# Kernel optimization log

Measured on AMD Instinct MI355X. Metric: run time of the kernel, lower is better.

Reference implementation:

```python
import jax, jax.numpy as jnp
import numpy as np

B, S, D = 4, 4096, 1024
H = 16
HD = D // H
L = 4
MLP_MULT = 4
MAX_CHUNKS = 1024
ROPE_BASE = 10000.0


def _rms(x):
    eps = jnp.asarray(jnp.finfo(x.dtype).eps, x.dtype)
    return x * jax.lax.rsqrt(jnp.mean(x * x, axis=-1, keepdims=True) + eps)


def _rope_tables(seq_len, dim):
    inv = 1.0 / ROPE_BASE ** (np.arange(0, dim, 2, dtype=np.float32) / dim)
    t = np.arange(seq_len, dtype=np.float32)
    freqs = np.outer(t, inv)  # [T, dim/2]
    return jnp.asarray(np.cos(freqs)), jnp.asarray(np.sin(freqs))


def _apply_rope(x, cos, sin):
    # x: [B,H,T,hd]; cos/sin: [T, hd/2]
    half = x.shape[-1] // 2
    x1, x2 = x[..., :half], x[..., half:]
    c = cos[None, None, :, :]
    s = sin[None, None, :, :]
    return jnp.concatenate([x1 * c + x2 * s, -x1 * s + x2 * c], axis=-1)


def chunk_reduce(x, boundary_hard, max_chunks):
    # x: [B,S,D]; boundary_hard: [B,S] in {0,1}, boundary_hard[:,0]==1
    ids = jnp.cumsum(boundary_hard.astype(jnp.int32), axis=1) - 1  # [B,S]
    seg = lambda xb, ib: jax.ops.segment_sum(xb, ib, num_segments=max_chunks)
    sums = jax.vmap(seg)(x, ids)                                   # [B,C,D]
    counts = jax.vmap(seg)(jnp.ones(x.shape[:2], x.dtype)[..., None].swapaxes(0, 0), ids) if False else jax.vmap(seg)(jnp.ones((x.shape[0], x.shape[1], 1), x.dtype), ids)
    latents = sums / jnp.maximum(counts, 1.0)
    num_chunks = ids[:, -1] + 1
    valid = jnp.arange(max_chunks)[None, :] < num_chunks[:, None]
    return latents, ids, valid


def _attn(x, wq, wk, wv, wo, qg, cos, sin):
    b, t, _ = x.shape
    q = (x @ wq.T).reshape(b, t, H, HD).transpose(0, 2, 1, 3)
    k = (x @ wk.T).reshape(b, t, H, HD).transpose(0, 2, 1, 3)
    v = (x @ wv.T).reshape(b, t, H, HD).transpose(0, 2, 1, 3)
    q = _apply_rope(_rms(q), cos, sin)
    k = _apply_rope(_rms(k), cos, sin)
    q = q * qg[None, :, None, None]
    scores = jnp.einsum('bhqd,bhkd->bhqk', q, k) / np.sqrt(HD).astype(np.float32)
    causal = jnp.tril(jnp.ones((t, t), bool))
    scores = jnp.where(causal[None, None], scores, jnp.asarray(-jnp.inf, scores.dtype))
    p = jax.nn.softmax(scores, axis=-1)
    y = jnp.einsum('bhqk,bhkd->bhqd', p, v).transpose(0, 2, 1, 3).reshape(b, t, D)
    return y @ wo.T


def _mlp(x, fc, proj):
    h = jax.nn.relu(x @ fc.T)
    return (h * h) @ proj.T


def reference(x, boundary_hard, Wq, Wk, Wv, Wo, q_gain, fc_w, proj_w,
              attn_scale, mlp_scale, resid_mix, max_chunks):
    latents, _, valid = chunk_reduce(x, boundary_hard, max_chunks)
    cos, sin = _rope_tables(max_chunks, HD)
    x0 = latents
    h = latents
    for l in range(L):
        mix = resid_mix[l]
        h = mix[0][None, None, :] * h + mix[1][None, None, :] * x0
        a = _attn(_rms(h), Wq[l], Wk[l], Wv[l], Wo[l], q_gain[l], cos, sin)
        h = h + attn_scale[l][None, None, :] * a
        h = h + mlp_scale[l][None, None, :] * _mlp(_rms(h), fc_w[l], proj_w[l])
    return h * valid[..., None].astype(h.dtype)


def setup_inputs() -> dict:
    key = jax.random.key(0)
    ks = jax.random.split(key, 12)
    rng = np.random.default_rng(0)
    boundary = np.zeros((B, S), np.int32)
    for b in range(B):
        kcnt = int(rng.integers(MAX_CHUNKS // 2, MAX_CHUNKS - 1))
        pos = rng.choice(S, size=kcnt, replace=False)
        boundary[b, pos] = 1
    boundary[:, 0] = 1
    sd = 0.02
    return {
        'x': jax.random.normal(ks[0], (B, S, D), jnp.float32),
        'boundary_hard': jnp.asarray(boundary),
        'Wq': jax.random.normal(ks[1], (L, D, D), jnp.float32) * sd,
        'Wk': jax.random.normal(ks[2], (L, D, D), jnp.float32) * sd,
        'Wv': jax.random.normal(ks[3], (L, D, D), jnp.float32) * sd,
        'Wo': jax.random.normal(ks[4], (L, D, D), jnp.float32) * sd,
        'q_gain': jnp.ones((L, H), jnp.float32),
        'fc_w': jax.random.normal(ks[5], (L, MLP_MULT * D, D), jnp.float32) * sd,
        'proj_w': jax.random.normal(ks[6], (L, D, MLP_MULT * D), jnp.float32) * sd,
        'attn_scale': jnp.ones((L, D), jnp.float32),
        'mlp_scale': jnp.ones((L, D), jnp.float32),
        'resid_mix': jnp.stack([jnp.ones((L, D)), jnp.zeros((L, D))], axis=1).astype(jnp.float32),
        'max_chunks': MAX_CHUNKS,
    }
```

## Files before the change

### kernel.cpp

```cpp
#include <hip/hip_runtime.h>
#include <math.h>

#define BB   4
#define SS   4096
#define DD   1024
#define HH   16
#define HDIM 64
#define CC   1024
#define DFF  4096
#define LL   4

static constexpr float F32_EPS = 1.1920928955078125e-07f;

typedef __attribute__((ext_vector_type(8))) __bf16 bf16x8;
typedef __attribute__((ext_vector_type(4))) float  f32x4;

__device__ __forceinline__ uint f2bf(float f) {
    uint u = __float_as_uint(f);
    return (u + 0x7fffu + ((u >> 16) & 1u)) >> 16;
}
__device__ __forceinline__ float bf2f(uint u) {
    return __uint_as_float(u << 16);
}

__device__ __forceinline__ void gl_lds16(const ushort* g, ushort* l) {
    __builtin_amdgcn_global_load_lds(
        (const __attribute__((address_space(1))) unsigned int*)g,
        (__attribute__((address_space(3))) unsigned int*)l, 16, 0, 0);
}

__global__ __launch_bounds__(256) void castlayer_kernel(const float* __restrict__ Wq,
                                                        const float* __restrict__ Wk,
                                                        const float* __restrict__ Wv,
                                                        const float* __restrict__ Wo,
                                                        const float* __restrict__ fc,
                                                        const float* __restrict__ proj,
                                                        ushort* __restrict__ out) {
    int i = blockIdx.x * blockDim.x + threadIdx.x;
    const int U = DD * DD / 8;
    const float* src;
    if (i < 3 * U) {
        src = (i < U ? Wq : (i < 2 * U ? Wk : Wv)) + (size_t)(i < U ? i : (i < 2*U ? i-U : i-2*U)) * 8;
    } else if (i < 4 * U) {
        src = Wo + (size_t)(i - 3 * U) * 8;
    } else if (i < 8 * U) {
        src = fc + (size_t)(i - 4 * U) * 8;
    } else {
        src = proj + (size_t)(i - 8 * U) * 8;
    }
    const float4* p = (const float4*)src;
    float4 a = p[0], b = p[1];
    uint4 o;
    o.x = f2bf(a.x) | (f2bf(a.y) << 16);
    o.y = f2bf(a.z) | (f2bf(a.w) << 16);
    o.z = f2bf(b.x) | (f2bf(b.y) << 16);
    o.w = f2bf(b.z) | (f2bf(b.w) << 16);
    *(uint4*)(out + (size_t)i * 8) = o;
}

__global__ void rope_init_kernel(float* __restrict__ cosT, float* __restrict__ sinT) {
    int idx = blockIdx.x * blockDim.x + threadIdx.x;
    int pos = idx >> 5;
    int i   = idx & 31;
    float inv = powf(10000.0f, -(float)i / 32.0f);
    float f = (float)pos * inv;
    cosT[idx] = cosf(f);
    sinT[idx] = sinf(f);
}

__global__ __launch_bounds__(1024) void scan_kernel(const int* __restrict__ boundary,
                                                    int* __restrict__ starts,
                                                    int* __restrict__ nch) {
    __shared__ int tmp[1024];
    int b = blockIdx.x, t = threadIdx.x;
    int base = b * SS + t * 4;
    int v0 = boundary[base + 0], v1 = boundary[base + 1];
    int v2 = boundary[base + 2], v3 = boundary[base + 3];
    int p0 = v0, p1 = p0 + v1, p2 = p1 + v2, p3 = p2 + v3;
    tmp[t] = p3;
    __syncthreads();
    for (int off = 1; off < 1024; off <<= 1) {
        int add = (t >= off) ? tmp[t - off] : 0;
        __syncthreads();
        tmp[t] += add;
        __syncthreads();
    }
    int excl = tmp[t] - p3;
    if (v0) starts[b * (CC + 1) + (excl + p0 - 1)] = t * 4 + 0;
    if (v1) starts[b * (CC + 1) + (excl + p1 - 1)] = t * 4 + 1;
    if (v2) starts[b * (CC + 1) + (excl + p2 - 1)] = t * 4 + 2;
    if (v3) starts[b * (CC + 1) + (excl + p3 - 1)] = t * 4 + 3;
    int total = tmp[1023];
    if (t == 0) nch[b] = total;
    for (int c = t; c <= CC; c += 1024)
        if (c >= total) starts[b * (CC + 1) + c] = SS;
}

__global__ __launch_bounds__(256) void latents_kernel(const float* __restrict__ x,
                                                      const int* __restrict__ starts,
                                                      float* __restrict__ h,
                                                      float* __restrict__ x0) {
    int c = blockIdx.x, b = blockIdx.y, t = threadIdx.x;
    int s0 = starts[b * (CC + 1) + c];
    int s1 = starts[b * (CC + 1) + c + 1];
    float a0 = 0.f, a1 = 0.f, a2 = 0.f, a3 = 0.f;
    for (int r = s0; r < s1; ++r) {
        const float4 xv = *(const float4*)&x[((size_t)(b * SS + r)) * DD + t * 4];
        a0 += xv.x; a1 += xv.y; a2 += xv.z; a3 += xv.w;
    }
    float inv = (s1 > s0) ? 1.0f / (float)(s1 - s0) : 0.0f;
    float4 o = make_float4(a0 * inv, a1 * inv, a2 * inv, a3 * inv);
    size_t off = ((size_t)(b * CC + c)) * DD + t * 4;
    *(float4*)&h[off]  = o;
    *(float4*)&x0[off] = o;
}

__global__ __launch_bounds__(256) void rmsmix_kernel(const float* __restrict__ hin,
                                                     const float* __restrict__ x0,
                                                     const float* __restrict__ mix,
                                                     float* __restrict__ hout,
                                                     ushort* __restrict__ xnout) {
    int row = blockIdx.x, t = threadIdx.x;
    size_t off = (size_t)row * DD + t * 4;
    float4 hv = *(const float4*)&hin[off];
    float4 m0 = *(const float4*)&mix[t * 4];
    float4 m1 = *(const float4*)&mix[DD + t * 4];
    float4 xv = *(const float4*)&x0[off];
    hv.x = m0.x * hv.x + m1.x * xv.x;
    hv.y = m0.y * hv.y + m1.y * xv.y;
    hv.z = m0.z * hv.z + m1.z * xv.z;
    hv.w = m0.w * hv.w + m1.w * xv.w;
    float ss = hv.x * hv.x + hv.y * hv.y + hv.z * hv.z + hv.w * hv.w;
    for (int o = 32; o; o >>= 1) ss += __shfl_xor(ss, o);
    __shared__ float wsum[4];
    int lane = t & 63, wid = t >> 6;
    if (lane == 0) wsum[wid] = ss;
    __syncthreads();
    float tot = wsum[0] + wsum[1] + wsum[2] + wsum[3];
    float r = rsqrtf(tot * (1.0f / DD) + F32_EPS);
    *(float4*)&hout[off] = hv;
    uint2 pk;
    pk.x = f2bf(hv.x * r) | (f2bf(hv.y * r) << 16);
    pk.y = f2bf(hv.z * r) | (f2bf(hv.w * r) << 16);
    *(uint2*)&xnout[off] = pk;
}

template <int HASMIX>
__global__ __launch_bounds__(256) void residrms_kernel(float* __restrict__ h,
                                                       const ushort* __restrict__ a0,
                                                       const ushort* __restrict__ a1,
                                                       const float* __restrict__ scale,
                                                       const float* __restrict__ x0,
                                                       const float* __restrict__ mix,
                                                       ushort* __restrict__ xnout) {
    int row = blockIdx.x, t = threadIdx.x;
    size_t off = (size_t)row * DD + t * 4;
    float4 hv = *(const float4*)&h[off];
    uint2 pa = *(const uint2*)&a0[off];
    uint2 pb = *(const uint2*)&a1[off];
    float4 sv = *(const float4*)&scale[t * 4];
    hv.x += sv.x * (bf2f(pa.x & 0xffff) + bf2f(pb.x & 0xffff));
    hv.y += sv.y * (bf2f(pa.x >> 16)    + bf2f(pb.x >> 16));
    hv.z += sv.z * (bf2f(pa.y & 0xffff) + bf2f(pb.y & 0xffff));
    hv.w += sv.w * (bf2f(pa.y >> 16)    + bf2f(pb.y >> 16));
    if (HASMIX) {
        float4 m0 = *(const float4*)&mix[t * 4];
        float4 m1 = *(const float4*)&mix[DD + t * 4];
        float4 xv = *(const float4*)&x0[off];
        hv.x = m0.x * hv.x + m1.x * xv.x;
        hv.y = m0.y * hv.y + m1.y * xv.y;
        hv.z = m0.z * hv.z + m1.z * xv.z;
        hv.w = m0.w * hv.w + m1.w * xv.w;
    }
    float ss = hv.x * hv.x + hv.y * hv.y + hv.z * hv.z + hv.w * hv.w;
    for (int o = 32; o; o >>= 1) ss += __shfl_xor(ss, o);
    __shared__ float wsum[4];
    int lane = t & 63, wid = t >> 6;
    if (lane == 0) wsum[wid] = ss;
    __syncthreads();
    float tot = wsum[0] + wsum[1] + wsum[2] + wsum[3];
    float r = rsqrtf(tot * (1.0f / DD) + F32_EPS);
    *(float4*)&h[off] = hv;
    uint2 pk;
    pk.x = f2bf(hv.x * r) | (f2bf(hv.y * r) << 16);
    pk.y = f2bf(hv.z * r) | (f2bf(hv.w * r) << 16);
    *(uint2*)&xnout[off] = pk;
}

template <int EPI>
__global__ __launch_bounds__(512) void gemm_bf16(const ushort* __restrict__ A,
                                                 const ushort* __restrict__ W,
                                                 ushort* __restrict__ C0,
                                                 ushort* __restrict__ C1,
                                                 ushort* __restrict__ C2,
                                                 const float* __restrict__ cosT,
                                                 const float* __restrict__ sinT,
                                                 const float* __restrict__ gain,
                                                 int M, int N, int K, int lda, int ldw,
                                                 size_t partStride) {
    __shared__ __align__(16) ushort Als[2][128 * 64];
    __shared__ __align__(16) ushort Wls[2][128 * 64];
    const int tid  = threadIdx.x;
    const int wid  = tid >> 6, lane = tid & 63;
    const int wr   = wid >> 1, wc   = wid & 1;
    const int l15  = lane & 15, lhi = lane >> 4;

    const int gx = gridDim.x, gy = gridDim.y;
    int i = (blockIdx.z * gy + blockIdx.y) * gx + blockIdx.x;
    int G = gx * gy * (int)gridDim.z;
    int v = (i & 7) * (G >> 3) + (i >> 3);
    int mt = v % gy;
    int rest = v / gy;
    int nt = rest % gx;
    int zt = rest / gx;
    const int mbase = mt * 128, nbase = nt * 128;

    A  += (size_t)zt * K;
    W  += (size_t)zt * K;
    C0 += (size_t)zt * partStride;

    const int srow8  = lane >> 3;
    const int gchunk = ((lane & 7) ^ srow8) * 8;
    const ushort* Ag = A + (size_t)(mbase + wid * 16 + srow8) * lda + gchunk;
    const ushort* Wg = W + (size_t)(nbase + wid * 16 + srow8) * ldw + gchunk;
    const int ldsoff = (wid * 16) * 64;

    f32x4 acc[2][4] = {};
    const int swz  = (l15 & 7) << 3;
    const int aoff = (wr * 32 + l15) * 64;
    const int woff = (wc * 64 + l15) * 64;

    auto STAGE = [&](ushort* Alb, ushort* Wlb, int kk) {
#pragma unroll
        for (int s = 0; s < 2; ++s) {
            gl_lds16(Ag + kk + (size_t)s * 8 * lda, Alb + ldsoff + s * 8 * 64);
            gl_lds16(Wg + kk + (size_t)s * 8 * ldw, Wlb + ldsoff + s * 8 * 64);
        }
    };
    auto COMPUTE = [&](const ushort* Ab, const ushort* Wb) {
#pragma unroll
        for (int ks = 0; ks < 2; ++ks) {
            const int fcol = (ks * 32 + lhi * 8) ^ swz;
            bf16x8 af[2], bfm[4];
#pragma unroll
            for (int m = 0; m < 2; ++m)
                af[m] = *(const bf16x8*)(Ab + aoff + m * 1024 + fcol);
#pragma unroll
            for (int n = 0; n < 4; ++n)
                bfm[n] = *(const bf16x8*)(Wb + woff + n * 1024 + fcol);
#pragma unroll
            for (int m = 0; m < 2; ++m)
#pragma unroll
                for (int n = 0; n < 4; ++n)
                    acc[m][n] = __builtin_amdgcn_mfma_f32_16x16x32_bf16(
                        af[m], bfm[n], acc[m][n], 0, 0, 0);
        }
    };

    STAGE(Als[0], Wls[0], 0);
    __syncthreads();
    for (int k0 = 0; k0 < K; k0 += 128) {
        if (k0 + 64 < K) STAGE(Als[1], Wls[1], k0 + 64);
        COMPUTE(Als[0], Wls[0]);
        __syncthreads();
        if (k0 + 128 < K) STAGE(Als[0], Wls[0], k0 + 128);
        COMPUTE(Als[1], Wls[1]);
        __syncthreads();
    }

    const int row0 = mbase + wr * 32 + lhi * 4;

    if (EPI == 3) {
        const int third = nbase >> 10;
        const int bandbase = (nbase & 1023) + wc * 64;
        ushort* dst = (third == 0) ? C0 : (third == 1 ? C1 : C2);
        if (third == 2) {
#pragma unroll
            for (int m = 0; m < 2; ++m)
#pragma unroll
                for (int n = 0; n < 4; ++n)
#pragma unroll
                    for (int r = 0; r < 4; ++r) {
                        int rr = row0 + m * 16 + r;
                        dst[(size_t)rr * 1024 + bandbase + n * 16 + l15] =
                            (ushort)f2bf(acc[m][n][r]);
                    }
        } else {
            const int hd = bandbase >> 6;
            const float g = (third == 0) ? gain[hd] * 0.125f : 1.0f;
#pragma unroll
            for (int m = 0; m < 2; ++m)
#pragma unroll
                for (int r = 0; r < 4; ++r) {
                    int rr = row0 + m * 16 + r;
                    float v0 = acc[m][0][r], v1 = acc[m][1][r];
                    float v2 = acc[m][2][r], v3 = acc[m][3][r];
                    float ss = v0 * v0 + v1 * v1 + v2 * v2 + v3 * v3;
#pragma unroll
                    for (int off = 1; off < 16; off <<= 1) ss += __shfl_xor(ss, off);
                    float rn = rsqrtf(ss * (1.0f / HDIM) + F32_EPS);
                    v0 *= rn; v1 *= rn; v2 *= rn; v3 *= rn;
                    int c = rr & (CC - 1);
                    float c0 = cosT[c * 32 + l15],      s0 = sinT[c * 32 + l15];
                    float c1 = cosT[c * 32 + 16 + l15], s1 = sinT[c * 32 + 16 + l15];
                    float o0 = (v0 * c0 + v2 * s0) * g;
                    float o1 = (v1 * c1 + v3 * s1) * g;
                    float o2 = (v2 * c0 - v0 * s0) * g;
                    float o3 = (v3 * c1 - v1 * s1) * g;
                    size_t rbase = (size_t)rr * 1024 + bandbase;
                    dst[rbase + l15]      = (ushort)f2bf(o0);
                    dst[rbase + 16 + l15] = (ushort)f2bf(o1);
                    dst[rbase + 32 + l15] = (ushort)f2bf(o2);
                    dst[rbase + 48 + l15] = (ushort)f2bf(o3);
                }
        }
    } else {
        const int col0 = nbase + wc * 64 + l15;
#pragma unroll
        for (int m = 0; m < 2; ++m)
#pragma unroll
            for (int n = 0; n < 4; ++n) {
                int cc = col0 + n * 16;
#pragma unroll
                for (int r = 0; r < 4; ++r) {
                    int rr = row0 + m * 16 + r;
                    float v2 = acc[m][n][r];
                    if (EPI == 1) { v2 = fmaxf(v2, 0.0f); v2 = v2 * v2; }
                    C0[(size_t)rr * N + cc] = (ushort)f2bf(v2);
                }
            }
    }
}

__global__ __launch_bounds__(256) void vtrans_kernel(const ushort* __restrict__ v,
                                                     ushort* __restrict__ vt) {
    __shared__ ushort Ls[64][72];
    int kt = blockIdx.x, head = blockIdx.y, b = blockIdx.z;
    int tid = threadIdx.x;
    int r = tid >> 3;
    int ch = (tid & 7) * 8;
#pragma unroll
    for (int s = 0; s < 2; ++s) {
        int kv = r + s * 32;
        int4 t4 = *(const int4*)&v[((size_t)(b * CC + kt * 64 + kv)) * DD + head * HDIM + ch];
        *(int4*)&Ls[kv][ch] = t4;
    }
    __syncthreads();
#pragma unroll
    for (int s = 0; s < 2; ++s) {
        int d = r + s * 32;
        ushort o[8];
#pragma unroll
        for (int j = 0; j < 8; ++j) o[j] = Ls[ch + j][d];
        *(int4*)&vt[((size_t)((b * HH + head) * HDIM + d)) * CC + kt * 64 + ch] = *(int4*)o;
    }
}

__global__ __launch_bounds__(512) void attn_mfma(const ushort* __restrict__ q,
                                                 const ushort* __restrict__ k,
                                                 const ushort* __restrict__ vt,
                                                 ushort* __restrict__ y,
                                                 const float* __restrict__ gain) {
    __shared__ __align__(16) ushort Qs[128 * 64];
    __shared__ __align__(16) ushort Ks[64 * 64];
    __shared__ __align__(16) ushort VT[64 * 64];
    __shared__ __align__(16) ushort Ps[128 * 64];
    const int qt = 7 - blockIdx.x;
    const int head = blockIdx.y, b = blockIdx.z;
    const int tid = threadIdx.x;
    const int wid = tid >> 6, lane = tid & 63;
    const int l15 = lane & 15, lhi = lane >> 4;
    const int wq0 = wid * 16;
    const int qbase = qt * 128;
    const float mstat = 8.0f * fabsf(gain[head]);

    const int srow = tid >> 3;
    const int scol = (tid & 7) * 8;

#pragma unroll
    for (int s = 0; s < 2; ++s) {
        int r = srow + s * 64;
        int4 t4 = *(const int4*)&q[((size_t)(b * CC + qbase + r)) * DD + head * HDIM + scol];
        *(int4*)&Qs[r * 64 + (scol ^ ((r & 7) << 3))] = t4;
    }

    f32x4 oacc[4] = {};
    float lpart[4] = {0.f, 0.f, 0.f, 0.f};

    const int NT = 2 * qt + 2;

    auto LOADK = [&](int4& kr, int4& vr, int kt_) {
        kr = *(const int4*)&k[((size_t)(b * CC + kt_ * 64 + srow)) * DD + head * HDIM + scol];
        vr = *(const int4*)&vt[((size_t)((b * HH + head) * HDIM + srow)) * CC + kt_ * 64 + scol];
    };
    auto WRITEK = [&](const int4& kr, const int4& vr) {
        *(int4*)&Ks[srow * 64 + (scol ^ ((srow & 7) << 3))] = kr;
        *(int4*)&VT[srow * 64 + (scol ^ ((srow & 7) << 3))] = vr;
    };
    auto TILE = [&](int kt) {
        f32x4 sac[4] = {};
        __builtin_amdgcn_s_setprio(1);
#pragma unroll
        for (int ks = 0; ks < 2; ++ks) {
            int dcol = ks * 32 + lhi * 8;
            int arow = wq0 + l15;
            bf16x8 af = *(const bf16x8*)&Qs[arow * 64 + (dcol ^ ((arow & 7) << 3))];
#pragma unroll
            for (int n = 0; n < 4; ++n) {
                int krow = n * 16 + l15;
                bf16x8 bfr = *(const bf16x8*)&Ks[krow * 64 + (dcol ^ ((krow & 7) << 3))];
                sac[n] = __builtin_amdgcn_mfma_f32_16x16x32_bf16(af, bfr, sac[n], 0, 0, 0);
            }
        }
        __builtin_amdgcn_s_setprio(0);

        if (kt >= 2 * qt) {
            const int kb0 = kt * 64;
#pragma unroll
            for (int r = 0; r < 4; ++r) {
                int qrow_g = qbase + wq0 + lhi * 4 + r;
                float p0 = __expf(sac[0][r] - mstat);
                float p1 = __expf(sac[1][r] - mstat);
                float p2 = __expf(sac[2][r] - mstat);
                float p3 = __expf(sac[3][r] - mstat);
                if (kb0 + l15      > qrow_g) p0 = 0.f;
                if (kb0 + 16 + l15 > qrow_g) p1 = 0.f;
                if (kb0 + 32 + l15 > qrow_g) p2 = 0.f;
                if (kb0 + 48 + l15 > qrow_g) p3 = 0.f;
                lpart[r] += (p0 + p1) + (p2 + p3);
                int qrow_l = wq0 + lhi * 4 + r;
                int pb = qrow_l * 64, sw = (qrow_l & 7) << 3;
                Ps[pb + ((l15)      ^ sw)] = (ushort)f2bf(p0);
                Ps[pb + ((16 + l15) ^ sw)] = (ushort)f2bf(p1);
                Ps[pb + ((32 + l15) ^ sw)] = (ushort)f2bf(p2);
                Ps[pb + ((48 + l15) ^ sw)] = (ushort)f2bf(p3);
            }
        } else {
#pragma unroll
            for (int r = 0; r < 4; ++r) {
                float p0 = __expf(sac[0][r] - mstat);
                float p1 = __expf(sac[1][r] - mstat);
                float p2 = __expf(sac[2][r] - mstat);
                float p3 = __expf(sac[3][r] - mstat);
                lpart[r] += (p0 + p1) + (p2 + p3);
                int qrow_l = wq0 + lhi * 4 + r;
                int pb = qrow_l * 64, sw = (qrow_l & 7) << 3;
                Ps[pb + ((l15)      ^ sw)] = (ushort)f2bf(p0);
                Ps[pb + ((16 + l15) ^ sw)] = (ushort)f2bf(p1);
                Ps[pb + ((32 + l15) ^ sw)] = (ushort)f2bf(p2);
                Ps[pb + ((48 + l15) ^ sw)] = (ushort)f2bf(p3);
            }
        }

        __builtin_amdgcn_s_setprio(1);
#pragma unroll
        for (int ks = 0; ks < 2; ++ks) {
            int kcol = ks * 32 + lhi * 8;
            int arow = wq0 + l15;
            bf16x8 pf = *(const bf16x8*)&Ps[arow * 64 + (kcol ^ ((arow & 7) << 3))];
#pragma unroll
            for (int n = 0; n < 4; ++n) {
                int vrow = n * 16 + l15;
                bf16x8 vf = *(const bf16x8*)&VT[vrow * 64 + (kcol ^ ((vrow & 7) << 3))];
                oacc[n] = __builtin_amdgcn_mfma_f32_16x16x32_bf16(pf, vf, oacc[n], 0, 0, 0);
            }
        }
        __builtin_amdgcn_s_setprio(0);
    };

    int4 kra, vra, krb, vrb;
    LOADK(kra, vra, 0);
    for (int kt = 0; kt < NT; kt += 2) {
        __syncthreads();
        WRITEK(kra, vra);
        __syncthreads();
        LOADK(krb, vrb, kt + 1);
        TILE(kt);
        __syncthreads();
        WRITEK(krb, vrb);
        __syncthreads();
        if (kt + 2 < NT) LOADK(kra, vra, kt + 2);
        TILE(kt + 1);
    }

#pragma unroll
    for (int r = 0; r < 4; ++r) {
        float ls = lpart[r];
#pragma unroll
        for (int off = 1; off < 16; off <<= 1) ls += __shfl_xor(ls, off);
        float inv = 1.0f / ls;
        int qrow_g = qbase + wq0 + lhi * 4 + r;
        size_t base = ((size_t)(b * CC + qrow_g)) * DD + head * HDIM;
#pragma unroll
        for (int n = 0; n < 4; ++n)
            y[base + n * 16 + l15] = (ushort)f2bf(oacc[n][r] * inv);
    }
}

__global__ void residmask_kernel(const float* __restrict__ h, const ushort* __restrict__ a0,
                                 const ushort* __restrict__ a1,
                                 const float* __restrict__ scale,
                                 const int* __restrict__ nch,
                                 float* __restrict__ out) {
    int idx = blockIdx.x * blockDim.x + threadIdx.x;
    size_t off = (size_t)idx * 4;
    int c = (idx >> 8) & (CC - 1);
    int b = idx >> 18;
    float4 hv = *(const float4*)&h[off];
    uint2 pa = *(const uint2*)&a0[off];
    uint2 pb = *(const uint2*)&a1[off];
    float4 sv = *(const float4*)&scale[(idx & 255) * 4];
    hv.x += sv.x * (bf2f(pa.x & 0xffff) + bf2f(pb.x & 0xffff));
    hv.y += sv.y * (bf2f(pa.x >> 16)    + bf2f(pb.x >> 16));
    hv.z += sv.z * (bf2f(pa.y & 0xffff) + bf2f(pb.y & 0xffff));
    hv.w += sv.w * (bf2f(pa.y >> 16)    + bf2f(pb.y >> 16));
    if (c >= nch[b]) hv = make_float4(0.f, 0.f, 0.f, 0.f);
    *(float4*)&out[off] = hv;
}

extern "C" void kernel_launch(void* const* d_in, const int* in_sizes, int n_in,
                              void* d_out, int out_size, void* d_ws, size_t ws_size,
                              hipStream_t stream) {
    const float* x        = (const float*)d_in[0];
    const int*   boundary = (const int*)d_in[1];
    const float* Wq       = (const float*)d_in[2];
    const float* Wk       = (const float*)d_in[3];
    const float* Wv       = (const float*)d_in[4];
    const float* Wo       = (const float*)d_in[5];
    const float* qg       = (const float*)d_in[6];
    const float* fcw      = (const float*)d_in[7];
    const float* projw    = (const float*)d_in[8];
    const float* ascale   = (const float*)d_in[9];
    const float* mscale   = (const float*)d_in[10];
    const float* rmix     = (const float*)d_in[11];
    float* out = (float*)d_out;

    const size_t NTOK = (size_t)BB * CC * DD;
    const size_t NHID = (size_t)BB * CC * DFF;
    const size_t D2   = (size_t)DD * DD;

    float* ws   = (float*)d_ws;
    float*  h    = ws;
    float*  x0   = h  + NTOK;
    float*  pbf  = x0 + NTOK;
    float*  spare= pbf + NTOK;
    ushort* xnb  = (ushort*)(spare + NTOK);
    ushort* ybf  = xnb + NTOK;
    ushort* hidb = ybf + NTOK;
    ushort* wbuf = hidb + NHID;
    ushort* vtb  = wbuf + NHID;
    float*  cosT = (float*)(vtb + NTOK);
    float*  sinT = cosT + (size_t)CC * 32;
    int*    starts = (int*)(sinT + (size_t)CC * 32);
    int*    nch    = starts + BB * (CC + 1);

    ushort* pb0 = (ushort*)pbf;
    ushort* pb1 = pb0 + NTOK;

    ushort* qbb = hidb;
    ushort* kbb = hidb + NTOK;
    ushort* vbb = hidb + 2 * NTOK;

    ushort* wqkv = wbuf;
    ushort* wwo  = wbuf + 3 * D2;
    ushort* wfc  = wbuf + 4 * D2;
    ushort* wpj  = wbuf + 8 * D2;

    const int M = BB * CC;
    const int CASTL = (int)(12 * D2 / 8 / 256);

    rope_init_kernel<<<CC * 32 / 256, 256, 0, stream>>>(cosT, sinT);
    scan_kernel<<<BB, 1024, 0, stream>>>(boundary, starts, nch);
    latents_kernel<<<dim3(CC, BB), 256, 0, stream>>>(x, starts, h, x0);
    rmsmix_kernel<<<M, 256, 0, stream>>>(h, x0, rmix, h, xnb);

    for (int l = 0; l < LL; ++l) {
        castlayer_kernel<<<CASTL, 256, 0, stream>>>(Wq + l * D2, Wk + l * D2, Wv + l * D2,
                                                    Wo + l * D2,
                                                    fcw + (size_t)l * DFF * DD,
                                                    projw + (size_t)l * DD * DFF, wbuf);
        gemm_bf16<3><<<dim3(3 * DD / 128, M / 128, 1), 512, 0, stream>>>(
            xnb, wqkv, qbb, kbb, vbb, cosT, sinT, qg + l * HH, M, 3 * DD, DD, DD, DD, 0);
        vtrans_kernel<<<dim3(CC / 64, HH, BB), 256, 0, stream>>>(vbb, vtb);
        attn_mfma<<<dim3(8, HH, BB), 512, 0, stream>>>(qbb, kbb, vtb, ybf, qg + l * HH);
        gemm_bf16<0><<<dim3(DD / 128, M / 128, 2), 512, 0, stream>>>(
            ybf, wwo, pb0, nullptr, nullptr, nullptr, nullptr, nullptr,
            M, DD, DD / 2, DD, DD, NTOK);
        residrms_kernel<0><<<M, 256, 0, stream>>>(h, pb0, pb1, ascale + l * DD,
                                                  nullptr, nullptr, xnb);
        gemm_bf16<1><<<dim3(DFF / 128, M / 128, 1), 512, 0, stream>>>(
            xnb, wfc, hidb, nullptr, nullptr, nullptr, nullptr, nullptr,
            M, DFF, DD, DD, DD, 0);
        gemm_bf16<0><<<dim3(DD / 128, M / 128, 2), 512, 0, stream>>>(
            hidb, wpj, pb0, nullptr, nullptr, nullptr, nullptr, nullptr,
            M, DD, DFF / 2, DFF, DFF, NTOK);
        if (l < LL - 1) {
            residrms_kernel<1><<<M, 256, 0, stream>>>(h, pb0, pb1, mscale + l * DD,
                                                      x0, rmix + (size_t)(l + 1) * 2 * DD, xnb);
        } else {
            residmask_kernel<<<(int)(NTOK / 4 / 256), 256, 0, stream>>>(
                h, pb0, pb1, mscale + l * DD, nch, out);
        }
    }
}
```

Baseline: 847.2 us.

## Widen attention KV tile to 128 keys per iteration

The chunk-attention kernel now processes 128 keys per loop iteration instead of 64. K, V^T and P shared buffers double in size, and the swizzle pattern widens to 16 rows. This halves the number of barrier pairs and loop iterations per query tile and doubles the MFMA work between syncs. In exchange it uses more LDS and registers, which may lower occupancy, and it applies the causal mask to a full 128-wide diagonal tile.

```diff
diff --git a/kernel.cpp b/kernel.cpp
--- a/kernel.cpp
+++ b/kernel.cpp
@@ -362,9 +362,9 @@
                                                  ushort* __restrict__ y,
                                                  const float* __restrict__ gain) {
     __shared__ __align__(16) ushort Qs[128 * 64];
-    __shared__ __align__(16) ushort Ks[64 * 64];
-    __shared__ __align__(16) ushort VT[64 * 64];
-    __shared__ __align__(16) ushort Ps[128 * 64];
+    __shared__ __align__(16) ushort Ks[128 * 64];
+    __shared__ __align__(16) ushort VT[64 * 128];
+    __shared__ __align__(16) ushort Ps[128 * 128];
     const int qt = 7 - blockIdx.x;
     const int head = blockIdx.y, b = blockIdx.z;
     const int tid = threadIdx.x;
@@ -387,18 +387,28 @@
     f32x4 oacc[4] = {};
     float lpart[4] = {0.f, 0.f, 0.f, 0.f};
 
-    const int NT = 2 * qt + 2;
-
-    auto LOADK = [&](int4& kr, int4& vr, int kt_) {
-        kr = *(const int4*)&k[((size_t)(b * CC + kt_ * 64 + srow)) * DD + head * HDIM + scol];
-        vr = *(const int4*)&vt[((size_t)((b * HH + head) * HDIM + srow)) * CC + kt_ * 64 + scol];
+    const int NT = qt + 1;
+
+    int4 kr[2], vr[2];
+    auto LOADK = [&](int kt_) {
+#pragma unroll
+        for (int s = 0; s < 2; ++s) {
+            kr[s] = *(const int4*)&k[((size_t)(b * CC + kt_ * 128 + srow + s * 64)) * DD
+                                     + head * HDIM + scol];
+            vr[s] = *(const int4*)&vt[((size_t)((b * HH + head) * HDIM + srow)) * CC
+                                      + kt_ * 128 + scol + s * 64];
+        }
     };
-    auto WRITEK = [&](const int4& kr, const int4& vr) {
-        *(int4*)&Ks[srow * 64 + (scol ^ ((srow & 7) << 3))] = kr;
-        *(int4*)&VT[srow * 64 + (scol ^ ((srow & 7) << 3))] = vr;
+    auto WRITEK = [&]() {
+#pragma unroll
+        for (int s = 0; s < 2; ++s) {
+            int r = srow + s * 64;
+            *(int4*)&Ks[r * 64 + (scol ^ ((r & 7) << 3))] = kr[s];
+            *(int4*)&VT[srow * 128 + ((scol + s * 64) ^ ((srow & 15) << 3))] = vr[s];
+        }
     };
     auto TILE = [&](int kt) {
-        f32x4 sac[4] = {};
+        f32x4 sac[8] = {};
         __builtin_amdgcn_s_setprio(1);
 #pragma unroll
         for (int ks = 0; ks < 2; ++ks) {
@@ -406,7 +416,7 @@
             int arow = wq0 + l15;
             bf16x8 af = *(const bf16x8*)&Qs[arow * 64 + (dcol ^ ((arow & 7) << 3))];
 #pragma unroll
-            for (int n = 0; n < 4; ++n) {
+            for (int n = 0; n < 8; ++n) {
                 int krow = n * 16 + l15;
                 bf16x8 bfr = *(const bf16x8*)&Ks[krow * 64 + (dcol ^ ((krow & 7) << 3))];
                 sac[n] = __builtin_amdgcn_mfma_f32_16x16x32_bf16(af, bfr, sac[n], 0, 0, 0);
@@ -414,73 +424,51 @@
         }
         __builtin_amdgcn_s_setprio(0);
 
-        if (kt >= 2 * qt) {
-            const int kb0 = kt * 64;
-#pragma unroll
-            for (int r = 0; r < 4; ++r) {
-                int qrow_g = qbase + wq0 + lhi * 4 + r;
-                float p0 = __expf(sac[0][r] - mstat);
-                float p1 = __expf(sac[1][r] - mstat);
-                float p2 = __expf(sac[2][r] - mstat);
-                float p3 = __expf(sac[3][r] - mstat);
-                if (kb0 + l15      > qrow_g) p0 = 0.f;
-                if (kb0 + 16 + l15 > qrow_g) p1 = 0.f;
-                if (kb0 + 32 + l15 > qrow_g) p2 = 0.f;
-                if (kb0 + 48 + l15 > qrow_g) p3 = 0.f;
-                lpart[r] += (p0 + p1) + (p2 + p3);
-                int qrow_l = wq0 + lhi * 4 + r;
-                int pb = qrow_l * 64, sw = (qrow_l & 7) << 3;
-                Ps[pb + ((l15)      ^ sw)] = (ushort)f2bf(p0);
-                Ps[pb + ((16 + l15) ^ sw)] = (ushort)f2bf(p1);
-                Ps[pb + ((32 + l15) ^ sw)] = (ushort)f2bf(p2);
-                Ps[pb + ((48 + l15) ^ sw)] = (ushort)f2bf(p3);
+        const bool diag = (kt == qt);
+        const int kb0 = kt * 128;
+#pragma unroll
+        for (int r = 0; r < 4; ++r) {
+            int qrow_l = wq0 + lhi * 4 + r;
+            int qrow_g = qbase + qrow_l;
+            float pv[8];
+            float sum = 0.f;
+#pragma unroll
+            for (int n = 0; n < 8; ++n) {
+                float p = __expf(sac[n][r] - mstat);
+                if (diag && (kb0 + n * 16 + l15) > qrow_g) p = 0.f;
+                pv[n] = p;
+                sum += p;
             }
-        } else {
-#pragma unroll
-            for (int r = 0; r < 4; ++r) {
-                float p0 = __expf(sac[0][r] - mstat);
-                float p1 = __expf(sac[1][r] - mstat);
-                float p2 = __expf(sac[2][r] - mstat);
-                float p3 = __expf(sac[3][r] - mstat);
-                lpart[r] += (p0 + p1) + (p2 + p3);
-                int qrow_l = wq0 + lhi * 4 + r;
-                int pb = qrow_l * 64, sw = (qrow_l & 7) << 3;
-                Ps[pb + ((l15)      ^ sw)] = (ushort)f2bf(p0);
-                Ps[pb + ((16 + l15) ^ sw)] = (ushort)f2bf(p1);
-                Ps[pb + ((32 + l15) ^ sw)] = (ushort)f2bf(p2);
-                Ps[pb + ((48 + l15) ^ sw)] = (ushort)f2bf(p3);
-            }
+            lpart[r] += sum;
+            int pb = qrow_l * 128, sw = (qrow_l & 15) << 3;
+#pragma unroll
+            for (int n = 0; n < 8; ++n)
+                Ps[pb + ((n * 16 + l15) ^ sw)] = (ushort)f2bf(pv[n]);
         }
 
         __builtin_amdgcn_s_setprio(1);
 #pragma unroll
-        for (int ks = 0; ks < 2; ++ks) {
+        for (int ks = 0; ks < 4; ++ks) {
             int kcol = ks * 32 + lhi * 8;
             int arow = wq0 + l15;
-            bf16x8 pf = *(const bf16x8*)&Ps[arow * 64 + (kcol ^ ((arow & 7) << 3))];
+            bf16x8 pf = *(const bf16x8*)&Ps[arow * 128 + (kcol ^ ((arow & 15) << 3))];
 #pragma unroll
             for (int n = 0; n < 4; ++n) {
                 int vrow = n * 16 + l15;
-                bf16x8 vf = *(const bf16x8*)&VT[vrow * 64 + (kcol ^ ((vrow & 7) << 3))];
+                bf16x8 vf = *(const bf16x8*)&VT[vrow * 128 + (kcol ^ ((vrow & 15) << 3))];
                 oacc[n] = __builtin_amdgcn_mfma_f32_16x16x32_bf16(pf, vf, oacc[n], 0, 0, 0);
             }
         }
         __builtin_amdgcn_s_setprio(0);
     };
 
-    int4 kra, vra, krb, vrb;
-    LOADK(kra, vra, 0);
-    for (int kt = 0; kt < NT; kt += 2) {
+    LOADK(0);
+    for (int kt = 0; kt < NT; ++kt) {
         __syncthreads();
-        WRITEK(kra, vra);
+        WRITEK();
         __syncthreads();
-        LOADK(krb, vrb, kt + 1);
+        if (kt + 1 < NT) LOADK(kt + 1);
         TILE(kt);
-        __syncthreads();
-        WRITEK(krb, vrb);
-        __syncthreads();
-        if (kt + 2 < NT) LOADK(kra, vra, kt + 2);
-        TILE(kt + 1);
     }
 
 #pragma unroll
```

Result: slower. 1.002 ms (+18.3%).

## Double-buffer K/V tiles in attention and store x0 residual as bf16

Applied to the files above, without the earlier changes.

The attention kernel now keeps two LDS buffers for the K and V^T tiles. The next tile is loaded from global memory and written to the spare buffer while the current one is computed, which cuts four barriers per two tiles down to one per tile. Separately, the x0 skip tensor is stored in bf16 instead of fp32, which halves its read and write traffic in the latents, rmsmix and residrms kernels. Storing x0 in bf16 loses precision in the residual mix, and the extra LDS raises shared-memory use per block, which may lower occupancy.

```diff
diff --git a/kernel.cpp b/kernel.cpp
--- a/kernel.cpp
+++ b/kernel.cpp
@@ -99,7 +99,7 @@
 __global__ __launch_bounds__(256) void latents_kernel(const float* __restrict__ x,
                                                       const int* __restrict__ starts,
                                                       float* __restrict__ h,
-                                                      float* __restrict__ x0) {
+                                                      ushort* __restrict__ x0) {
     int c = blockIdx.x, b = blockIdx.y, t = threadIdx.x;
     int s0 = starts[b * (CC + 1) + c];
     int s1 = starts[b * (CC + 1) + c + 1];
@@ -109,14 +109,17 @@
         a0 += xv.x; a1 += xv.y; a2 += xv.z; a3 += xv.w;
     }
     float inv = (s1 > s0) ? 1.0f / (float)(s1 - s0) : 0.0f;
-    float4 o = make_float4(a0 * inv, a1 * inv, a2 * inv, a3 * inv);
+    a0 *= inv; a1 *= inv; a2 *= inv; a3 *= inv;
     size_t off = ((size_t)(b * CC + c)) * DD + t * 4;
-    *(float4*)&h[off]  = o;
-    *(float4*)&x0[off] = o;
+    *(float4*)&h[off] = make_float4(a0, a1, a2, a3);
+    uint2 pk;
+    pk.x = f2bf(a0) | (f2bf(a1) << 16);
+    pk.y = f2bf(a2) | (f2bf(a3) << 16);
+    *(uint2*)&x0[off] = pk;
 }
 
 __global__ __launch_bounds__(256) void rmsmix_kernel(const float* __restrict__ hin,
-                                                     const float* __restrict__ x0,
+                                                     const ushort* __restrict__ x0,
                                                      const float* __restrict__ mix,
                                                      float* __restrict__ hout,
                                                      ushort* __restrict__ xnout) {
@@ -125,11 +128,11 @@
     float4 hv = *(const float4*)&hin[off];
     float4 m0 = *(const float4*)&mix[t * 4];
     float4 m1 = *(const float4*)&mix[DD + t * 4];
-    float4 xv = *(const float4*)&x0[off];
-    hv.x = m0.x * hv.x + m1.x * xv.x;
-    hv.y = m0.y * hv.y + m1.y * xv.y;
-    hv.z = m0.z * hv.z + m1.z * xv.z;
-    hv.w = m0.w * hv.w + m1.w * xv.w;
+    uint2 xv = *(const uint2*)&x0[off];
+    hv.x = m0.x * hv.x + m1.x * bf2f(xv.x & 0xffff);
+    hv.y = m0.y * hv.y + m1.y * bf2f(xv.x >> 16);
+    hv.z = m0.z * hv.z + m1.z * bf2f(xv.y & 0xffff);
+    hv.w = m0.w * hv.w + m1.w * bf2f(xv.y >> 16);
     float ss = hv.x * hv.x + hv.y * hv.y + hv.z * hv.z + hv.w * hv.w;
     for (int o = 32; o; o >>= 1) ss += __shfl_xor(ss, o);
     __shared__ float wsum[4];
@@ -150,7 +153,7 @@
                                                        const ushort* __restrict__ a0,
                                                        const ushort* __restrict__ a1,
                                                        const float* __restrict__ scale,
-                                                       const float* __restrict__ x0,
+                                                       const ushort* __restrict__ x0,
                                                        const float* __restrict__ mix,
                                                        ushort* __restrict__ xnout) {
     int row = blockIdx.x, t = threadIdx.x;
@@ -166,11 +169,11 @@
     if (HASMIX) {
         float4 m0 = *(const float4*)&mix[t * 4];
         float4 m1 = *(const float4*)&mix[DD + t * 4];
-        float4 xv = *(const float4*)&x0[off];
-        hv.x = m0.x * hv.x + m1.x * xv.x;
-        hv.y = m0.y * hv.y + m1.y * xv.y;
-        hv.z = m0.z * hv.z + m1.z * xv.z;
-        hv.w = m0.w * hv.w + m1.w * xv.w;
+        uint2 xv = *(const uint2*)&x0[off];
+        hv.x = m0.x * hv.x + m1.x * bf2f(xv.x & 0xffff);
+        hv.y = m0.y * hv.y + m1.y * bf2f(xv.x >> 16);
+        hv.z = m0.z * hv.z + m1.z * bf2f(xv.y & 0xffff);
+        hv.w = m0.w * hv.w + m1.w * bf2f(xv.y >> 16);
     }
     float ss = hv.x * hv.x + hv.y * hv.y + hv.z * hv.z + hv.w * hv.w;
     for (int o = 32; o; o >>= 1) ss += __shfl_xor(ss, o);
@@ -362,8 +365,8 @@
                                                  ushort* __restrict__ y,
                                                  const float* __restrict__ gain) {
     __shared__ __align__(16) ushort Qs[128 * 64];
-    __shared__ __align__(16) ushort Ks[64 * 64];
-    __shared__ __align__(16) ushort VT[64 * 64];
+    __shared__ __align__(16) ushort Ks[2][64 * 64];
+    __shared__ __align__(16) ushort VT[2][64 * 64];
     __shared__ __align__(16) ushort Ps[128 * 64];
     const int qt = 7 - blockIdx.x;
     const int head = blockIdx.y, b = blockIdx.z;
@@ -389,15 +392,18 @@
 
     const int NT = 2 * qt + 2;
 
-    auto LOADK = [&](int4& kr, int4& vr, int kt_) {
+    int4 kr, vr;
+    auto LOADK = [&](int kt_) {
         kr = *(const int4*)&k[((size_t)(b * CC + kt_ * 64 + srow)) * DD + head * HDIM + scol];
         vr = *(const int4*)&vt[((size_t)((b * HH + head) * HDIM + srow)) * CC + kt_ * 64 + scol];
     };
-    auto WRITEK = [&](const int4& kr, const int4& vr) {
-        *(int4*)&Ks[srow * 64 + (scol ^ ((srow & 7) << 3))] = kr;
-        *(int4*)&VT[srow * 64 + (scol ^ ((srow & 7) << 3))] = vr;
+    auto WRITEK = [&](int buf) {
+        *(int4*)&Ks[buf][srow * 64 + (scol ^ ((srow & 7) << 3))] = kr;
+        *(int4*)&VT[buf][srow * 64 + (scol ^ ((srow & 7) << 3))] = vr;
     };
-    auto TILE = [&](int kt) {
+    auto TILE = [&](int kt, int buf) {
+        const ushort* Kb = Ks[buf];
+        const ushort* Vb = VT[buf];
         f32x4 sac[4] = {};
         __builtin_amdgcn_s_setprio(1);
 #pragma unroll
@@ -408,7 +414,7 @@
 #pragma unroll
             for (int n = 0; n < 4; ++n) {
                 int krow = n * 16 + l15;
-                bf16x8 bfr = *(const bf16x8*)&Ks[krow * 64 + (dcol ^ ((krow & 7) << 3))];
+                bf16x8 bfr = *(const bf16x8*)&Kb[krow * 64 + (dcol ^ ((krow & 7) << 3))];
                 sac[n] = __builtin_amdgcn_mfma_f32_16x16x32_bf16(af, bfr, sac[n], 0, 0, 0);
             }
         }
@@ -461,26 +467,20 @@
 #pragma unroll
             for (int n = 0; n < 4; ++n) {
                 int vrow = n * 16 + l15;
-                bf16x8 vf = *(const bf16x8*)&VT[vrow * 64 + (kcol ^ ((vrow & 7) << 3))];
+                bf16x8 vf = *(const bf16x8*)&Vb[vrow * 64 + (kcol ^ ((vrow & 7) << 3))];
                 oacc[n] = __builtin_amdgcn_mfma_f32_16x16x32_bf16(pf, vf, oacc[n], 0, 0, 0);
             }
         }
         __builtin_amdgcn_s_setprio(0);
     };
 
-    int4 kra, vra, krb, vrb;
-    LOADK(kra, vra, 0);
-    for (int kt = 0; kt < NT; kt += 2) {
+    LOADK(0);
+    WRITEK(0);
+    for (int kt = 0; kt < NT; ++kt) {
+        if (kt + 1 < NT) LOADK(kt + 1);
         __syncthreads();
-        WRITEK(kra, vra);
-        __syncthreads();
-        LOADK(krb, vrb, kt + 1);
-        TILE(kt);
-        __syncthreads();
-        WRITEK(krb, vrb);
-        __syncthreads();
-        if (kt + 2 < NT) LOADK(kra, vra, kt + 2);
-        TILE(kt + 1);
+        TILE(kt, kt & 1);
+        if (kt + 1 < NT) WRITEK((kt + 1) & 1);
     }
 
 #pragma unroll
@@ -539,12 +539,11 @@
     const size_t NHID = (size_t)BB * CC * DFF;
     const size_t D2   = (size_t)DD * DD;
 
-    float* ws   = (float*)d_ws;
-    float*  h    = ws;
-    float*  x0   = h  + NTOK;
-    float*  pbf  = x0 + NTOK;
-    float*  spare= pbf + NTOK;
-    ushort* xnb  = (ushort*)(spare + NTOK);
+    float*  h    = (float*)d_ws;
+    ushort* x0b  = (ushort*)(h + NTOK);
+    ushort* pb0  = x0b + NTOK;
+    ushort* pb1  = pb0 + NTOK;
+    ushort* xnb  = pb1 + NTOK;
     ushort* ybf  = xnb + NTOK;
     ushort* hidb = ybf + NTOK;
     ushort* wbuf = hidb + NHID;
@@ -554,9 +553,6 @@
     int*    starts = (int*)(sinT + (size_t)CC * 32);
     int*    nch    = starts + BB * (CC + 1);
 
-    ushort* pb0 = (ushort*)pbf;
-    ushort* pb1 = pb0 + NTOK;
-
     ushort* qbb = hidb;
     ushort* kbb = hidb + NTOK;
     ushort* vbb = hidb + 2 * NTOK;
@@ -571,8 +567,8 @@
 
     rope_init_kernel<<<CC * 32 / 256, 256, 0, stream>>>(cosT, sinT);
     scan_kernel<<<BB, 1024, 0, stream>>>(boundary, starts, nch);
-    latents_kernel<<<dim3(CC, BB), 256, 0, stream>>>(x, starts, h, x0);
-    rmsmix_kernel<<<M, 256, 0, stream>>>(h, x0, rmix, h, xnb);
+    latents_kernel<<<dim3(CC, BB), 256, 0, stream>>>(x, starts, h, x0b);
+    rmsmix_kernel<<<M, 256, 0, stream>>>(h, x0b, rmix, h, xnb);
 
     for (int l = 0; l < LL; ++l) {
         castlayer_kernel<<<CASTL, 256, 0, stream>>>(Wq + l * D2, Wk + l * D2, Wv + l * D2,
@@ -596,7 +592,7 @@
             M, DD, DFF / 2, DFF, DFF, NTOK);
         if (l < LL - 1) {
             residrms_kernel<1><<<M, 256, 0, stream>>>(h, pb0, pb1, mscale + l * DD,
-                                                      x0, rmix + (size_t)(l + 1) * 2 * DD, xnb);
+                                                      x0b, rmix + (size_t)(l + 1) * 2 * DD, xnb);
         } else {
             residmask_kernel<<<(int)(NTOK / 4 / 256), 256, 0, stream>>>(
                 h, pb0, pb1, mscale + l * DD, nch, out);
```

Result: no change. 844.4 us (-0.3%).
